# Performance work log

Measured on AMD Instinct MI355X. Metric: run time of the kernel, lower is better.

## Reference

```python
import jax, jax.numpy as jnp
import numpy as np

D_MODEL = 512
N_EXPERTS = 8
HIDDEN = D_MODEL * 4
EPS = 1e-10

def setup_inputs() -> dict:
    key = jax.random.key(0)
    ks = jax.random.split(key, 8)
    B, N = 4, 2048
    T = B * N
    x = jax.random.normal(ks[0], (B, N, D_MODEL), dtype=jnp.float32)
    u = jax.random.uniform(ks[1], (T, N_EXPERTS), dtype=jnp.float32, minval=1e-6, maxval=1.0)
    s_in = 1.0 / np.sqrt(D_MODEL)
    s_h = 1.0 / np.sqrt(HIDDEN)
    router_w = jax.random.uniform(ks[2], (D_MODEL, N_EXPERTS), jnp.float32, -s_in, s_in)
    router_b = jax.random.uniform(ks[3], (N_EXPERTS,), jnp.float32, -s_in, s_in)
    w1 = jax.random.uniform(ks[4], (N_EXPERTS, D_MODEL, HIDDEN), jnp.float32, -s_in, s_in)
    b1 = jax.random.uniform(ks[5], (N_EXPERTS, HIDDEN), jnp.float32, -s_in, s_in)
    w2 = jax.random.uniform(ks[6], (N_EXPERTS, HIDDEN, D_MODEL), jnp.float32, -s_h, s_h)
    b2 = jax.random.uniform(ks[7], (N_EXPERTS, D_MODEL), jnp.float32, -s_h, s_h)
    return {"x": x, "u": u, "router_w": router_w, "router_b": router_b,
            "w1": w1, "b1": b1, "w2": w2, "b2": b2}

def reference(x, u, router_w, router_b, w1, b1, w2, b2):
    B, N, d = x.shape
    x_flat = x.reshape(-1, d)  # (T, d)
    logits = x_flat @ router_w + router_b  # (T, E)
    # Gumbel-softmax, tau=1.0, hard=True (straight-through)
    g = -jnp.log(-jnp.log(u) + EPS)
    y_soft = jax.nn.softmax(logits + g, axis=-1)
    idx = jnp.argmax(y_soft, axis=-1)
    hard = jax.nn.one_hot(idx, logits.shape[-1], dtype=y_soft.dtype)
    weights = hard - jax.lax.stop_gradient(y_soft) + y_soft  # (T, E)
    # aux load-balancing loss
    probs = jax.nn.softmax(logits, axis=-1)
    importance = probs.sum(axis=0) / jnp.maximum(jnp.float32(logits.shape[0]), 1.0)
    target = 1.0 / logits.shape[-1]
    aux_loss = jnp.mean((importance - target) ** 2)
    # all-expert dense compute then weighted combine
    h = jax.nn.gelu(jnp.einsum('td,edh->eth', x_flat, w1) + b1[:, None, :], approximate=False)
    expert_outputs = jnp.einsum('eth,ehd->etd', h, w2) + b2[:, None, :]  # (E, T, d)
    output = jnp.einsum('te,etd->td', weights, expert_outputs)
    return output.reshape(B, N, d), aux_loss
```

## Files before the change

kernel.cpp:

```cpp
#include <hip/hip_runtime.h>
#include <stdint.h>
#include <math.h>

#define NUM_TOK 8192
#define DM 512
#define NE 8
#define NH 2048
#define MAX_TILES 72
#define NBLK 32

typedef float f32x4 __attribute__((ext_vector_type(4)));
typedef __bf16 bf16x8 __attribute__((ext_vector_type(8)));

#define WS_COUNTS   0
#define WS_OFFSETS  64
#define WS_IMP      96
#define WS_TILE_E   128
#define WS_TILE_R0  416
#define WS_EXP      704
#define WS_WTOK     33472
#define WS_PERM     66240
#define WS_XG       99008
#define WS_H        8618688
#define WS_W1T      42697408
#define WS_W2T      59474624
#define WS_PROBS    WS_XG
#define WS_RANK     WS_H
#define WS_BHIST    (WS_H + 32768)
#define WS_BBASE    (WS_H + 33792)

__device__ __forceinline__ uint16_t f2bf(float f) {
  union { float f; uint32_t u; } c; c.f = f;
  return (uint16_t)((c.u + 0x7FFFu + ((c.u >> 16) & 1u)) >> 16);
}

__device__ __forceinline__ float gelu_fast(float v) {
  float z = 1.5957691216f * v * (1.0f + 0.044715f * v * v);
  float em = __expf(-z);
  return v / (1.0f + em);
}

__device__ __forceinline__ void gload_lds16(const void* g, void* l) {
  __builtin_amdgcn_global_load_lds(
      (const __attribute__((address_space(1))) uint32_t*)g,
      (__attribute__((address_space(3))) uint32_t*)l, 16, 0, 0);
}

#define WAIT_BARRIER(N) asm volatile("s_waitcnt vmcnt(" #N ")\ns_barrier" ::: "memory")
#define RAW_BARRIER()   asm volatile("s_barrier" ::: "memory")

__global__ __launch_bounds__(256) void k_router(
    const float* __restrict__ x, const float* __restrict__ u,
    const float* __restrict__ rw, const float* __restrict__ rb,
    int* __restrict__ expert_of, float* __restrict__ wtok,
    float* __restrict__ probs)
{
  int wv = threadIdx.x >> 6, lane = threadIdx.x & 63;
  int t = blockIdx.x * 4 + wv;

  const float4* xr = (const float4*)(x + (size_t)t * DM + lane * 8);
  float4 xa = xr[0], xb = xr[1];
  float xs[8] = {xa.x, xa.y, xa.z, xa.w, xb.x, xb.y, xb.z, xb.w};

  double acc[NE];
  #pragma unroll
  for (int e = 0; e < NE; ++e) acc[e] = 0.0;
  #pragma unroll
  for (int j = 0; j < 8; ++j) {
    const float4* rr = (const float4*)(rw + (size_t)(lane * 8 + j) * NE);
    float4 r0 = rr[0], r1 = rr[1];
    double xv = (double)xs[j];
    acc[0] += xv * (double)r0.x; acc[1] += xv * (double)r0.y;
    acc[2] += xv * (double)r0.z; acc[3] += xv * (double)r0.w;
    acc[4] += xv * (double)r1.x; acc[5] += xv * (double)r1.y;
    acc[6] += xv * (double)r1.z; acc[7] += xv * (double)r1.w;
  }
  #pragma unroll
  for (int m = 1; m < 64; m <<= 1) {
    #pragma unroll
    for (int e = 0; e < NE; ++e) acc[e] += __shfl_xor(acc[e], m, 64);
  }
  double lg[NE];
  #pragma unroll
  for (int e = 0; e < NE; ++e) lg[e] = acc[e] + (double)rb[e];

  int le = lane & 7;
  double lgE = le == 0 ? lg[0] : le == 1 ? lg[1] : le == 2 ? lg[2] : le == 3 ? lg[3]
             : le == 4 ? lg[4] : le == 5 ? lg[5] : le == 6 ? lg[6] : lg[7];

  double yE = -1e300;
  if (lane < 8) {
    double uv = (double)u[(size_t)t * NE + lane];
    double g = -log(-log(uv) + 1e-10);
    yE = lgE + g;
  }
  double ymax = yE;
  #pragma unroll
  for (int m = 1; m < 8; m <<= 1) ymax = fmax(ymax, __shfl_xor(ymax, m, 64));
  double ex = (lane < 8) ? exp(yE - ymax) : 0.0;
  double s = ex;
  #pragma unroll
  for (int m = 1; m < 8; m <<= 1) s += __shfl_xor(s, m, 64);
  double p = 1.0 / s;
  unsigned long long mk = __ballot(lane < 8 && yE == ymax);
  int sel = __ffsll(mk) - 1;

  double lm = lgE;
  #pragma unroll
  for (int m = 1; m < 8; m <<= 1) lm = fmax(lm, __shfl_xor(lm, m, 64));
  double pr = exp(lgE - lm);
  double ssum = pr;
  #pragma unroll
  for (int m = 1; m < 8; m <<= 1) ssum += __shfl_xor(ssum, m, 64);

  if (lane < 8) probs[(size_t)t * NE + lane] = (float)(pr / ssum);
  if (lane == 0) {
    expert_of[t] = sel;
    wtok[t] = (float)((1.0 - p) + p);
  }
}

__global__ __launch_bounds__(256) void k_postroute(
    const int* __restrict__ expert_of, const float* __restrict__ probs,
    int* __restrict__ rank_local, int* __restrict__ block_hist,
    float* __restrict__ imp)
{
  __shared__ int whist[4][8];
  __shared__ float simp[4][8];
  int tid = threadIdx.x, lane = tid & 63, wid = tid >> 6;
  int t = blockIdx.x * 256 + tid;
  int sel = expert_of[t];

  int cnt[8]; int lrank = 0;
  unsigned long long below = (1ull << lane) - 1ull;
  #pragma unroll
  for (int e = 0; e < 8; ++e) {
    unsigned long long m = __ballot(sel == e);
    cnt[e] = (int)__popcll(m);
    if (e == sel) lrank = (int)__popcll(m & below);
  }
  if (lane == 0) {
    #pragma unroll
    for (int e = 0; e < 8; ++e) whist[wid][e] = cnt[e];
  }

  const float4* pp = (const float4*)(probs + (size_t)t * NE);
  float4 pa = pp[0], pb = pp[1];
  float ps[8] = {pa.x, pa.y, pa.z, pa.w, pb.x, pb.y, pb.z, pb.w};
  #pragma unroll
  for (int j = 0; j < 8; ++j) {
    float v = ps[j];
    #pragma unroll
    for (int m = 1; m < 64; m <<= 1) v += __shfl_xor(v, m, 64);
    if (lane == 0) simp[wid][j] = v;
  }
  __syncthreads();

  int base = 0;
  #pragma unroll
  for (int w = 0; w < 4; ++w) if (w < wid) base += whist[w][sel];
  rank_local[t] = base + lrank;

  if (tid < 8) {
    int c = whist[0][tid] + whist[1][tid] + whist[2][tid] + whist[3][tid];
    block_hist[blockIdx.x * 8 + tid] = c;
    float sv = simp[0][tid] + simp[1][tid] + simp[2][tid] + simp[3][tid];
    atomicAdd(&imp[tid], sv);
  }
}

__global__ __launch_bounds__(256) void k_offsets(
    const int* __restrict__ block_hist, const float* __restrict__ imp,
    int* __restrict__ counts, int* __restrict__ offsets,
    int* __restrict__ block_base, float* __restrict__ aux_out,
    int* __restrict__ tile_e, int* __restrict__ tile_r0)
{
  __shared__ int sh[NBLK * 8];
  __shared__ int scnt[8];
  __shared__ int soff[8];
  __shared__ float simp[8];
  int tid = threadIdx.x;

  sh[tid] = block_hist[tid];
  if (tid < 8) simp[tid] = imp[tid];
  __syncthreads();

  if (tid < 8) {
    int c = 0;
    #pragma unroll
    for (int b = 0; b < NBLK; ++b) c += sh[b * 8 + tid];
    scnt[tid] = c;
    counts[tid] = c;
  }
  __syncthreads();

  if (tid == 0) {
    int o = 0;
    #pragma unroll
    for (int e = 0; e < NE; ++e) { soff[e] = o; offsets[e] = o; o += scnt[e]; }
    float a = 0.0f;
    #pragma unroll
    for (int e = 0; e < NE; ++e) {
      float dv = simp[e] / 8192.0f - 0.125f;
      a += dv * dv;
    }
    aux_out[0] = a / 8.0f;
    int nt = 0;
    for (int e = 0; e < NE; ++e) {
      int ntile = (scnt[e] + 127) >> 7;
      for (int j = 0; j < ntile; ++j) { tile_e[nt] = e; tile_r0[nt] = soff[e] + j * 128; ++nt; }
    }
    for (int i = nt; i < MAX_TILES; ++i) { tile_e[i] = -1; tile_r0[i] = 0; }
  }
  __syncthreads();

  int b = tid >> 3, e = tid & 7;
  int run = soff[e];
  for (int bp = 0; bp < b; ++bp) run += sh[bp * 8 + e];
  block_base[tid] = run;
}

__global__ __launch_bounds__(256) void k_scatter2(
    const int* __restrict__ expert_of, const int* __restrict__ rank_local,
    const int* __restrict__ block_base, int* __restrict__ perm)
{
  int t = blockIdx.x * 256 + threadIdx.x;
  int e = expert_of[t];
  perm[block_base[blockIdx.x * 8 + e] + rank_local[t]] = t;
}

__global__ __launch_bounds__(64) void k_gather(
    const float* __restrict__ x, const int* __restrict__ perm, uint16_t* __restrict__ Xg)
{
  int r = blockIdx.x;
  int lane = threadIdx.x;
  int t = perm[r];
  const float4* src = (const float4*)(x + (size_t)t * DM);
  float4 a = src[lane * 2];
  float4 b = src[lane * 2 + 1];
  uint32_t p0 = (uint32_t)f2bf(a.x) | ((uint32_t)f2bf(a.y) << 16);
  uint32_t p1 = (uint32_t)f2bf(a.z) | ((uint32_t)f2bf(a.w) << 16);
  uint32_t p2 = (uint32_t)f2bf(b.x) | ((uint32_t)f2bf(b.y) << 16);
  uint32_t p3 = (uint32_t)f2bf(b.z) | ((uint32_t)f2bf(b.w) << 16);
  uint4 v = make_uint4(p0, p1, p2, p3);
  ((uint4*)(Xg + (size_t)r * DM))[lane] = v;
}

__global__ __launch_bounds__(256) void k_transpose_bf16(
    const float* __restrict__ src, uint16_t* __restrict__ dst, int K, int N)
{
  __shared__ float T[64][65];
  int e = blockIdx.z;
  const float* s = src + (size_t)e * K * N;
  uint16_t* d = dst + (size_t)e * K * N;
  int n0 = blockIdx.x * 64, k0 = blockIdx.y * 64;
  int tid = threadIdx.x;
  int tr = tid >> 4;
  int tc = (tid & 15) * 4;
  #pragma unroll
  for (int p = 0; p < 4; ++p) {
    int k = tr + p * 16;
    float4 v = *(const float4*)(s + (size_t)(k0 + k) * N + n0 + tc);
    T[k][tc] = v.x; T[k][tc + 1] = v.y; T[k][tc + 2] = v.z; T[k][tc + 3] = v.w;
  }
  __syncthreads();
  #pragma unroll
  for (int p = 0; p < 2; ++p) {
    int slot = p * 256 + tid;
    int n = slot >> 3;
    int c = (slot & 7) * 8;
    uint16_t tmp[8];
    #pragma unroll
    for (int j = 0; j < 8; ++j) tmp[j] = f2bf(T[c + j][n]);
    *(uint4*)(d + (size_t)(n0 + n) * K + k0 + c) = *(uint4*)tmp;
  }
}

__device__ __forceinline__ void mfma_128x128(
    const uint16_t* Asb, const uint16_t* Bsb, f32x4 (&acc)[4][4],
    int wm, int wn, int l16, int quad)
{
  #pragma unroll
  for (int ks = 0; ks < 2; ++ks) {
    bf16x8 a[4], b[4];
    #pragma unroll
    for (int mi = 0; mi < 4; ++mi) {
      int row = wm * 64 + mi * 16 + l16;
      a[mi] = *(const bf16x8*)(Asb + row * 64 + (((ks * 4 + quad) ^ (l16 & 7)) * 8));
    }
    #pragma unroll
    for (int ni = 0; ni < 4; ++ni) {
      int row = wn * 64 + ni * 16 + l16;
      b[ni] = *(const bf16x8*)(Bsb + row * 64 + (((ks * 4 + quad) ^ (l16 & 7)) * 8));
    }
    #pragma unroll
    for (int mi = 0; mi < 4; ++mi)
      #pragma unroll
      for (int ni = 0; ni < 4; ++ni)
        acc[mi][ni] = __builtin_amdgcn_mfma_f32_16x16x32_bf16(a[mi], b[ni], acc[mi][ni], 0, 0, 0);
  }
}

__global__ __launch_bounds__(256) void k_ffn1(
    const uint16_t* __restrict__ Xg, const uint16_t* __restrict__ w1t,
    const float* __restrict__ b1,
    const int* __restrict__ offsets, const int* __restrict__ counts,
    const int* __restrict__ tile_e, const int* __restrict__ tile_r0,
    uint16_t* __restrict__ hbuf)
{
  int w = (blockIdx.x & 7) * (MAX_TILES * 16 / 8) + (blockIdx.x >> 3);
  int tile = w >> 4;
  int cb = w & 15;
  int e = tile_e[tile];
  if (e < 0) return;
  int row0 = tile_r0[tile];
  int row_end = offsets[e] + counts[e];
  int n0 = cb * 128;
  const uint16_t* Bt = w1t + (size_t)e * DM * NH;

  __shared__ uint16_t As[2][128 * 64];
  __shared__ uint16_t Bs[2][128 * 64];

  int tid = threadIdx.x;
  int lane = tid & 63, wid = tid >> 6;
  int wm = wid >> 1, wn = wid & 1;
  int l16 = lane & 15, quad = lane >> 4;

  int lrow = lane >> 3;
  int lsw  = (lane & 7) ^ lrow;
  const uint16_t *ga[4], *gb[4];
  int lo[4];
  #pragma unroll
  for (int j = 0; j < 4; ++j) {
    int r = wid * 32 + j * 8;
    ga[j] = Xg + (size_t)(row0 + r + lrow) * DM + lsw * 8;
    gb[j] = Bt + (size_t)(n0 + r + lrow) * DM + lsw * 8;
    lo[j] = r * 64;
  }

  #define FFN1_ISSUE(B) do { \
    _Pragma("unroll") for (int j = 0; j < 4; ++j) { gload_lds16(ga[j], As[B] + lo[j]); ga[j] += 64; } \
    _Pragma("unroll") for (int j = 0; j < 4; ++j) { gload_lds16(gb[j], Bs[B] + lo[j]); gb[j] += 64; } \
  } while (0)

  f32x4 acc[4][4] = {};

  FFN1_ISSUE(0);
  FFN1_ISSUE(1);
  #pragma unroll 2
  for (int k = 0; k < 8; ++k) {
    if (k < 7) WAIT_BARRIER(8); else WAIT_BARRIER(0);
    int b = k & 1;
    mfma_128x128(As[b], Bs[b], acc, wm, wn, l16, quad);
    RAW_BARRIER();
    if (k < 6) { if (b) FFN1_ISSUE(1); else FFN1_ISSUE(0); }
  }

  #pragma unroll
  for (int ni = 0; ni < 4; ++ni) {
    int col = n0 + wn * 64 + ni * 16 + l16;
    float bv = b1[e * NH + col];
    #pragma unroll
    for (int mi = 0; mi < 4; ++mi) {
      int rbase = wm * 64 + mi * 16 + quad * 4;
      #pragma unroll
      for (int r = 0; r < 4; ++r) {
        int grow = row0 + rbase + r;
        if (grow < row_end) {
          float v = acc[mi][ni][r] + bv;
          hbuf[(size_t)grow * NH + col] = f2bf(gelu_fast(v));
        }
      }
    }
  }
}

__global__ __launch_bounds__(256) void k_ffn2(
    const uint16_t* __restrict__ hbuf, const uint16_t* __restrict__ w2t,
    const float* __restrict__ b2,
    const int* __restrict__ offsets, const int* __restrict__ counts,
    const int* __restrict__ tile_e, const int* __restrict__ tile_r0,
    const int* __restrict__ perm, const float* __restrict__ wtok,
    float* __restrict__ out)
{
  int w = (blockIdx.x & 7) * (MAX_TILES * 4 / 8) + (blockIdx.x >> 3);
  int tile = w >> 2;
  int cb = w & 3;
  int e = tile_e[tile];
  if (e < 0) return;
  int row0 = tile_r0[tile];
  int row_end = offsets[e] + counts[e];
  int n0 = cb * 128;
  const uint16_t* Bt = w2t + (size_t)e * NH * DM;

  __shared__ uint16_t As[2][128 * 64];
  __shared__ uint16_t Bs[2][128 * 64];

  int tid = threadIdx.x;
  int lane = tid & 63, wid = tid >> 6;
  int wm = wid >> 1, wn = wid & 1;
  int l16 = lane & 15, quad = lane >> 4;

  int lrow = lane >> 3;
  int lsw  = (lane & 7) ^ lrow;
  const uint16_t *ga[4], *gb[4];
  int lo[4];
  #pragma unroll
  for (int j = 0; j < 4; ++j) {
    int r = wid * 32 + j * 8;
    ga[j] = hbuf + (size_t)(row0 + r + lrow) * NH + lsw * 8;
    gb[j] = Bt + (size_t)(n0 + r + lrow) * NH + lsw * 8;
    lo[j] = r * 64;
  }

  #define FFN2_ISSUE(B) do { \
    _Pragma("unroll") for (int j = 0; j < 4; ++j) { gload_lds16(ga[j], As[B] + lo[j]); ga[j] += 64; } \
    _Pragma("unroll") for (int j = 0; j < 4; ++j) { gload_lds16(gb[j], Bs[B] + lo[j]); gb[j] += 64; } \
  } while (0)

  f32x4 acc[4][4] = {};

  FFN2_ISSUE(0);
  FFN2_ISSUE(1);
  #pragma unroll 2
  for (int k = 0; k < 32; ++k) {
    if (k < 31) WAIT_BARRIER(8); else WAIT_BARRIER(0);
    int b = k & 1;
    mfma_128x128(As[b], Bs[b], acc, wm, wn, l16, quad);
    RAW_BARRIER();
    if (k < 30) { if (b) FFN2_ISSUE(1); else FFN2_ISSUE(0); }
  }

  #pragma unroll
  for (int ni = 0; ni < 4; ++ni) {
    int col = n0 + wn * 64 + ni * 16 + l16;
    float bv = b2[e * DM + col];
    #pragma unroll
    for (int mi = 0; mi < 4; ++mi) {
      int rbase = wm * 64 + mi * 16 + quad * 4;
      #pragma unroll
      for (int r = 0; r < 4; ++r) {
        int grow = row0 + rbase + r;
        if (grow < row_end) {
          int tk = perm[grow];
          float wt = wtok[tk];
          out[(size_t)tk * DM + col] = (acc[mi][ni][r] + bv) * wt;
        }
      }
    }
  }
}

extern "C" void kernel_launch(void* const* d_in, const int* in_sizes, int n_in,
                              void* d_out, int out_size, void* d_ws, size_t ws_size,
                              hipStream_t stream)
{
  const float* x  = (const float*)d_in[0];
  const float* u  = (const float*)d_in[1];
  const float* rw = (const float*)d_in[2];
  const float* rb = (const float*)d_in[3];
  const float* w1 = (const float*)d_in[4];
  const float* b1 = (const float*)d_in[5];
  const float* w2 = (const float*)d_in[6];
  const float* b2 = (const float*)d_in[7];
  float* out = (float*)d_out;

  char* ws = (char*)d_ws;
  int*      counts     = (int*)(ws + WS_COUNTS);
  int*      offsets    = (int*)(ws + WS_OFFSETS);
  float*    imp        = (float*)(ws + WS_IMP);
  int*      tile_e     = (int*)(ws + WS_TILE_E);
  int*      tile_r0    = (int*)(ws + WS_TILE_R0);
  int*      expert_of  = (int*)(ws + WS_EXP);
  float*    wtok       = (float*)(ws + WS_WTOK);
  int*      perm       = (int*)(ws + WS_PERM);
  float*    probs      = (float*)(ws + WS_PROBS);
  int*      rank_local = (int*)(ws + WS_RANK);
  int*      block_hist = (int*)(ws + WS_BHIST);
  int*      block_base = (int*)(ws + WS_BBASE);
  uint16_t* Xg         = (uint16_t*)(ws + WS_XG);
  uint16_t* hbuf       = (uint16_t*)(ws + WS_H);
  uint16_t* w1t        = (uint16_t*)(ws + WS_W1T);
  uint16_t* w2t        = (uint16_t*)(ws + WS_W2T);

  hipMemsetAsync(d_ws, 0, 128, stream);
  k_transpose_bf16<<<dim3(NH / 64, DM / 64, NE), 256, 0, stream>>>(w1, w1t, DM, NH);
  k_transpose_bf16<<<dim3(DM / 64, NH / 64, NE), 256, 0, stream>>>(w2, w2t, NH, DM);
  k_router<<<NUM_TOK / 4, 256, 0, stream>>>(x, u, rw, rb, expert_of, wtok, probs);
  k_postroute<<<NBLK, 256, 0, stream>>>(expert_of, probs, rank_local, block_hist, imp);
  k_offsets<<<1, 256, 0, stream>>>(block_hist, imp, counts, offsets, block_base,
                                   out + (size_t)NUM_TOK * DM, tile_e, tile_r0);
  k_scatter2<<<NBLK, 256, 0, stream>>>(expert_of, rank_local, block_base, perm);
  k_gather<<<NUM_TOK, 64, 0, stream>>>(x, perm, Xg);
  k_ffn1<<<dim3(MAX_TILES * 16), 256, 0, stream>>>(Xg, w1t, b1, offsets, counts, tile_e, tile_r0, hbuf);
  k_ffn2<<<dim3(MAX_TILES * 4), 256, 0, stream>>>(hbuf, w2t, b2, offsets, counts, tile_e, tile_r0, perm, wtok, out);
}
```

Measured before the change: 291.6 us.

## Use 256-row expert tiles with 8 waves and triple-buffered LDS pipeline

Expert row tiles grow from 128 to 256 tokens, so each expert weight tile loaded into LDS is reused across twice as many rows. Both FFN kernels now run 8 waves per block. The double-buffered loop, which needed two barriers per step, becomes a three-stage buffer with one barrier per step, and the next load is issued before the current MFMA step. The two weight transpose launches are merged into one kernel. The cost is about 147KB of LDS per block and fewer blocks to spread across CUs, and ragged expert tails now waste up to 255 padding rows instead of 127.

After: 303.5 us. 1.04x slower.

```diff
diff --git a/kernel.cpp b/kernel.cpp
--- a/kernel.cpp
+++ b/kernel.cpp
@@ -6,7 +6,7 @@
 #define DM 512
 #define NE 8
 #define NH 2048
-#define MAX_TILES 72
+#define MAX_TILES 40
 #define NBLK 32
 
 typedef float f32x4 __attribute__((ext_vector_type(4)));
@@ -47,7 +47,6 @@
 }
 
 #define WAIT_BARRIER(N) asm volatile("s_waitcnt vmcnt(" #N ")\ns_barrier" ::: "memory")
-#define RAW_BARRIER()   asm volatile("s_barrier" ::: "memory")
 
 __global__ __launch_bounds__(256) void k_router(
     const float* __restrict__ x, const float* __restrict__ u,
@@ -207,8 +206,8 @@
     aux_out[0] = a / 8.0f;
     int nt = 0;
     for (int e = 0; e < NE; ++e) {
-      int ntile = (scnt[e] + 127) >> 7;
-      for (int j = 0; j < ntile; ++j) { tile_e[nt] = e; tile_r0[nt] = soff[e] + j * 128; ++nt; }
+      int ntile = (scnt[e] + 255) >> 8;
+      for (int j = 0; j < ntile; ++j) { tile_e[nt] = e; tile_r0[nt] = soff[e] + j * 256; ++nt; }
     }
     for (int i = nt; i < MAX_TILES; ++i) { tile_e[i] = -1; tile_r0[i] = 0; }
   }
@@ -246,14 +245,20 @@
   ((uint4*)(Xg + (size_t)r * DM))[lane] = v;
 }
 
-__global__ __launch_bounds__(256) void k_transpose_bf16(
-    const float* __restrict__ src, uint16_t* __restrict__ dst, int K, int N)
+__global__ __launch_bounds__(256) void k_transpose_both(
+    const float* __restrict__ w1, const float* __restrict__ w2,
+    uint16_t* __restrict__ w1t, uint16_t* __restrict__ w2t)
 {
   __shared__ float T[64][65];
-  int e = blockIdx.z;
+  int id = blockIdx.x;
+  const float* src; uint16_t* dst; int K, N, nx, rid;
+  if (id < 2048) { src = w1; dst = w1t; K = DM; N = NH; nx = NH / 64; rid = id; }
+  else           { src = w2; dst = w2t; K = NH; N = DM; nx = DM / 64; rid = id - 2048; }
+  int e = rid >> 8;
+  int r = rid & 255;
+  int n0 = (r % nx) * 64, k0 = (r / nx) * 64;
   const float* s = src + (size_t)e * K * N;
   uint16_t* d = dst + (size_t)e * K * N;
-  int n0 = blockIdx.x * 64, k0 = blockIdx.y * 64;
   int tid = threadIdx.x;
   int tr = tid >> 4;
   int tc = (tid & 15) * 4;
@@ -276,7 +281,7 @@
   }
 }
 
-__device__ __forceinline__ void mfma_128x128(
+__device__ __forceinline__ void mfma_256x128(
     const uint16_t* Asb, const uint16_t* Bsb, f32x4 (&acc)[4][4],
     int wm, int wn, int l16, int quad)
 {
@@ -301,16 +306,15 @@
   }
 }
 
-__global__ __launch_bounds__(256) void k_ffn1(
+__global__ __launch_bounds__(512) void k_ffn1(
     const uint16_t* __restrict__ Xg, const uint16_t* __restrict__ w1t,
     const float* __restrict__ b1,
     const int* __restrict__ offsets, const int* __restrict__ counts,
     const int* __restrict__ tile_e, const int* __restrict__ tile_r0,
     uint16_t* __restrict__ hbuf)
 {
-  int w = (blockIdx.x & 7) * (MAX_TILES * 16 / 8) + (blockIdx.x >> 3);
-  int tile = w >> 4;
-  int cb = w & 15;
+  int w = (blockIdx.x & 7) * (640 / 8) + (blockIdx.x >> 3);
+  int tile = w >> 4, cb = w & 15;
   int e = tile_e[tile];
   if (e < 0) return;
   int row0 = tile_r0[tile];
@@ -318,8 +322,8 @@
   int n0 = cb * 128;
   const uint16_t* Bt = w1t + (size_t)e * DM * NH;
 
-  __shared__ uint16_t As[2][128 * 64];
-  __shared__ uint16_t Bs[2][128 * 64];
+  __shared__ uint16_t As[3][256 * 64];
+  __shared__ uint16_t Bs[3][128 * 64];
 
   int tid = threadIdx.x;
   int lane = tid & 63, wid = tid >> 6;
@@ -328,32 +332,35 @@
 
   int lrow = lane >> 3;
   int lsw  = (lane & 7) ^ lrow;
-  const uint16_t *ga[4], *gb[4];
-  int lo[4];
+  const uint16_t *ga[4], *gb[2];
+  int loa[4], lob[2];
   #pragma unroll
   for (int j = 0; j < 4; ++j) {
     int r = wid * 32 + j * 8;
     ga[j] = Xg + (size_t)(row0 + r + lrow) * DM + lsw * 8;
+    loa[j] = r * 64;
+  }
+  #pragma unroll
+  for (int j = 0; j < 2; ++j) {
+    int r = wid * 16 + j * 8;
     gb[j] = Bt + (size_t)(n0 + r + lrow) * DM + lsw * 8;
-    lo[j] = r * 64;
+    lob[j] = r * 64;
   }
 
   #define FFN1_ISSUE(B) do { \
-    _Pragma("unroll") for (int j = 0; j < 4; ++j) { gload_lds16(ga[j], As[B] + lo[j]); ga[j] += 64; } \
-    _Pragma("unroll") for (int j = 0; j < 4; ++j) { gload_lds16(gb[j], Bs[B] + lo[j]); gb[j] += 64; } \
+    _Pragma("unroll") for (int j = 0; j < 4; ++j) { gload_lds16(ga[j], As[B] + loa[j]); ga[j] += 64; } \
+    _Pragma("unroll") for (int j = 0; j < 2; ++j) { gload_lds16(gb[j], Bs[B] + lob[j]); gb[j] += 64; } \
   } while (0)
 
   f32x4 acc[4][4] = {};
 
   FFN1_ISSUE(0);
   FFN1_ISSUE(1);
-  #pragma unroll 2
   for (int k = 0; k < 8; ++k) {
-    if (k < 7) WAIT_BARRIER(8); else WAIT_BARRIER(0);
-    int b = k & 1;
-    mfma_128x128(As[b], Bs[b], acc, wm, wn, l16, quad);
-    RAW_BARRIER();
-    if (k < 6) { if (b) FFN1_ISSUE(1); else FFN1_ISSUE(0); }
+    if (k < 7) WAIT_BARRIER(6); else WAIT_BARRIER(0);
+    int b3 = k % 3;
+    if (k < 6) { int nb = (k + 2) % 3; FFN1_ISSUE(nb); }
+    mfma_256x128(As[b3], Bs[b3], acc, wm, wn, l16, quad);
   }
 
   #pragma unroll
@@ -375,7 +382,7 @@
   }
 }
 
-__global__ __launch_bounds__(256) void k_ffn2(
+__global__ __launch_bounds__(512) void k_ffn2(
     const uint16_t* __restrict__ hbuf, const uint16_t* __restrict__ w2t,
     const float* __restrict__ b2,
     const int* __restrict__ offsets, const int* __restrict__ counts,
@@ -383,9 +390,8 @@
     const int* __restrict__ perm, const float* __restrict__ wtok,
     float* __restrict__ out)
 {
-  int w = (blockIdx.x & 7) * (MAX_TILES * 4 / 8) + (blockIdx.x >> 3);
-  int tile = w >> 2;
-  int cb = w & 3;
+  int w = (blockIdx.x & 7) * (160 / 8) + (blockIdx.x >> 3);
+  int tile = w >> 2, cb = w & 3;
   int e = tile_e[tile];
   if (e < 0) return;
   int row0 = tile_r0[tile];
@@ -393,8 +399,8 @@
   int n0 = cb * 128;
   const uint16_t* Bt = w2t + (size_t)e * NH * DM;
 
-  __shared__ uint16_t As[2][128 * 64];
-  __shared__ uint16_t Bs[2][128 * 64];
+  __shared__ uint16_t As[3][256 * 64];
+  __shared__ uint16_t Bs[3][128 * 64];
 
   int tid = threadIdx.x;
   int lane = tid & 63, wid = tid >> 6;
@@ -403,32 +409,35 @@
 
   int lrow = lane >> 3;
   int lsw  = (lane & 7) ^ lrow;
-  const uint16_t *ga[4], *gb[4];
-  int lo[4];
+  const uint16_t *ga[4], *gb[2];
+  int loa[4], lob[2];
   #pragma unroll
   for (int j = 0; j < 4; ++j) {
     int r = wid * 32 + j * 8;
     ga[j] = hbuf + (size_t)(row0 + r + lrow) * NH + lsw * 8;
+    loa[j] = r * 64;
+  }
+  #pragma unroll
+  for (int j = 0; j < 2; ++j) {
+    int r = wid * 16 + j * 8;
     gb[j] = Bt + (size_t)(n0 + r + lrow) * NH + lsw * 8;
-    lo[j] = r * 64;
+    lob[j] = r * 64;
   }
 
   #define FFN2_ISSUE(B) do { \
-    _Pragma("unroll") for (int j = 0; j < 4; ++j) { gload_lds16(ga[j], As[B] + lo[j]); ga[j] += 64; } \
-    _Pragma("unroll") for (int j = 0; j < 4; ++j) { gload_lds16(gb[j], Bs[B] + lo[j]); gb[j] += 64; } \
+    _Pragma("unroll") for (int j = 0; j < 4; ++j) { gload_lds16(ga[j], As[B] + loa[j]); ga[j] += 64; } \
+    _Pragma("unroll") for (int j = 0; j < 2; ++j) { gload_lds16(gb[j], Bs[B] + lob[j]); gb[j] += 64; } \
   } while (0)
 
   f32x4 acc[4][4] = {};
 
   FFN2_ISSUE(0);
   FFN2_ISSUE(1);
-  #pragma unroll 2
   for (int k = 0; k < 32; ++k) {
-    if (k < 31) WAIT_BARRIER(8); else WAIT_BARRIER(0);
-    int b = k & 1;
-    mfma_128x128(As[b], Bs[b], acc, wm, wn, l16, quad);
-    RAW_BARRIER();
-    if (k < 30) { if (b) FFN2_ISSUE(1); else FFN2_ISSUE(0); }
+    if (k < 31) WAIT_BARRIER(6); else WAIT_BARRIER(0);
+    int b3 = k % 3;
+    if (k < 30) { int nb = (k + 2) % 3; FFN2_ISSUE(nb); }
+    mfma_256x128(As[b3], Bs[b3], acc, wm, wn, l16, quad);
   }
 
   #pragma unroll
@@ -484,14 +493,13 @@
   uint16_t* w2t        = (uint16_t*)(ws + WS_W2T);
 
   hipMemsetAsync(d_ws, 0, 128, stream);
-  k_transpose_bf16<<<dim3(NH / 64, DM / 64, NE), 256, 0, stream>>>(w1, w1t, DM, NH);
-  k_transpose_bf16<<<dim3(DM / 64, NH / 64, NE), 256, 0, stream>>>(w2, w2t, NH, DM);
+  k_transpose_both<<<dim3(4096), 256, 0, stream>>>(w1, w2, w1t, w2t);
   k_router<<<NUM_TOK / 4, 256, 0, stream>>>(x, u, rw, rb, expert_of, wtok, probs);
   k_postroute<<<NBLK, 256, 0, stream>>>(expert_of, probs, rank_local, block_hist, imp);
   k_offsets<<<1, 256, 0, stream>>>(block_hist, imp, counts, offsets, block_base,
                                    out + (size_t)NUM_TOK * DM, tile_e, tile_r0);
   k_scatter2<<<NBLK, 256, 0, stream>>>(expert_of, rank_local, block_base, perm);
   k_gather<<<NUM_TOK, 64, 0, stream>>>(x, perm, Xg);
-  k_ffn1<<<dim3(MAX_TILES * 16), 256, 0, stream>>>(Xg, w1t, b1, offsets, counts, tile_e, tile_r0, hbuf);
-  k_ffn2<<<dim3(MAX_TILES * 4), 256, 0, stream>>>(hbuf, w2t, b2, offsets, counts, tile_e, tile_r0, perm, wtok, out);
-}
+  k_ffn1<<<dim3(640), 512, 0, stream>>>(Xg, w1t, b1, offsets, counts, tile_e, tile_r0, hbuf);
+  k_ffn2<<<dim3(160), 512, 0, stream>>>(hbuf, w2t, b2, offsets, counts, tile_e, tile_r0, perm, wtok, out);
+}
```
